# Kernel tuning notes

Measured on AMD Instinct MI355X. Metric: run time of the kernel, lower is better.

## Reference

```python
import jax, jax.numpy as jnp
import numpy as np

N = 100000   # number of points
K = 256      # num_clusters
F = 256      # num_features


def setup_inputs() -> dict:
    key = jax.random.key(0)
    k1, k2 = jax.random.split(key)
    x = jax.random.normal(k1, (1, N, F), dtype=jnp.float32)
    cluster_centers = jax.random.normal(k2, (K, F), dtype=jnp.float32)
    return {"x": x, "cluster_centers": cluster_centers}


def reference(x, cluster_centers):
    # x: (1, n, F); cluster_centers: (K, F)
    # Euclidean distances (1, n, K) via expansion (same math as norm of diff,
    # without materializing the (1, n, K, F) intermediate the torch code builds).
    x_sq = jnp.sum(x * x, axis=-1)                              # (1, n)
    c_sq = jnp.sum(cluster_centers * cluster_centers, axis=-1)  # (K,)
    cross = jnp.einsum('bnf,kf->bnk', x, cluster_centers)       # (1, n, K)
    d2 = x_sq[..., None] + c_sq[None, None, :] - 2.0 * cross
    distances = jnp.sqrt(jnp.maximum(d2, 0.0))                  # (1, n, K)
    # For each cluster, index of the nearest point (argmin over n).
    indices = jnp.argmin(distances, axis=1)                     # (1, K)
    # Gather the features of the nearest point per cluster.
    selected = jnp.take_along_axis(x, indices[:, :, None], axis=1)  # (1, K, F)
    return selected
```

## Files before the change

kernel.cpp:

```cpp
#include <hip/hip_runtime.h>
#include <stdint.h>

#define N_PTS 100000
#define K_CL  256
#define F_DIM 256
#define XROW  264

using bf16x8 = __attribute__((ext_vector_type(8))) short;
using f32x4  = __attribute__((ext_vector_type(4))) float;
typedef unsigned long long u64;

__device__ __forceinline__ unsigned short f32_to_bf16_rne(float f) {
    unsigned u = __float_as_uint(f);
    unsigned r = u + 0x7FFFu + ((u >> 16) & 1u);
    return (unsigned short)(r >> 16);
}

__global__ void prep_kernel(const float* __restrict__ c,
                            unsigned short* __restrict__ ch,
                            unsigned short* __restrict__ cl,
                            float* __restrict__ csq,
                            u64* __restrict__ best) {
    const int k = blockIdx.x;
    const int lane = threadIdx.x;
    float4 v = *(const float4*)(c + (size_t)k * F_DIM + lane * 4);

    float e[4] = {v.x, v.y, v.z, v.w};
    unsigned short hh[4], ll[4];
    #pragma unroll
    for (int i = 0; i < 4; ++i) {
        hh[i] = f32_to_bf16_rne(e[i]);
        float hf = __uint_as_float((unsigned)hh[i] << 16);
        ll[i] = f32_to_bf16_rne(e[i] - hf);
    }
    *(ushort4*)(ch + (size_t)k * F_DIM + lane * 4) = make_ushort4(hh[0], hh[1], hh[2], hh[3]);
    *(ushort4*)(cl + (size_t)k * F_DIM + lane * 4) = make_ushort4(ll[0], ll[1], ll[2], ll[3]);

    float s = v.x * v.x;
    s = fmaf(v.y, v.y, s);
    s = fmaf(v.z, v.z, s);
    s = fmaf(v.w, v.w, s);
    #pragma unroll
    for (int off = 32; off; off >>= 1) s += __shfl_down(s, off, 64);
    if (lane == 0) { csq[k] = s; best[k] = 0xFFFFFFFFFFFFFFFFULL; }
}

__global__ __launch_bounds__(512, 4)
void cluster_argmin_kernel(const float* __restrict__ x,
                           const unsigned short* __restrict__ ch,
                           const unsigned short* __restrict__ cl,
                           const float* __restrict__ csq,
                           u64* __restrict__ best) {
    __shared__ unsigned short xh_lds[64][XROW];
    __shared__ unsigned short xl_lds[64][XROW];
    __shared__ float xsq_lds[64];

    const int tid  = threadIdx.x;
    const int lane = tid & 63;
    const int w    = __builtin_amdgcn_readfirstlane(tid >> 6);
    const int n0   = blockIdx.x * 64;
    const int r15  = lane & 15;
    const int kg   = lane >> 4;

    const int col = lane * 4;
    #pragma unroll
    for (int i = 0; i < 8; ++i) {
        const int row = w + i * 8;
        int gr = n0 + row; if (gr > N_PTS - 1) gr = N_PTS - 1;
        float4 v = *(const float4*)(x + (size_t)gr * F_DIM + col);
        unsigned short h4[4], l4[4];
        float e[4] = {v.x, v.y, v.z, v.w};
        float s = 0.f;
        #pragma unroll
        for (int j = 0; j < 4; ++j) {
            h4[j] = f32_to_bf16_rne(e[j]);
            float hf = __uint_as_float((unsigned)h4[j] << 16);
            l4[j] = f32_to_bf16_rne(e[j] - hf);
            s = fmaf(e[j], e[j], s);
        }
        *(ushort4*)&xh_lds[row][col] = make_ushort4(h4[0], h4[1], h4[2], h4[3]);
        *(ushort4*)&xl_lds[row][col] = make_ushort4(l4[0], l4[1], l4[2], l4[3]);
        #pragma unroll
        for (int off = 32; off; off >>= 1) s += __shfl_xor(s, off, 64);
        if (lane == 0) xsq_lds[row] = s;
    }
    __syncthreads();

    const int kb = w * 32;
    const unsigned short* cbh[2];
    const unsigned short* cbl[2];
    #pragma unroll
    for (int cg = 0; cg < 2; ++cg) {
        size_t off = (size_t)(kb + cg * 16 + r15) * F_DIM + kg * 8;
        cbh[cg] = ch + off;
        cbl[cg] = cl + off;
    }

    f32x4 acc[4][2];
    #pragma unroll
    for (int pg = 0; pg < 4; ++pg)
        #pragma unroll
        for (int cg = 0; cg < 2; ++cg)
            acc[pg][cg] = (f32x4){0.f, 0.f, 0.f, 0.f};

    #pragma unroll 2
    for (int it = 0; it < 8; ++it) {
        const int f0 = it * 32;
        bf16x8 bh[2], bl[2];
        #pragma unroll
        for (int cg = 0; cg < 2; ++cg) {
            bh[cg] = *(const bf16x8*)(cbh[cg] + f0);
            bl[cg] = *(const bf16x8*)(cbl[cg] + f0);
        }
        #pragma unroll
        for (int pg = 0; pg < 4; ++pg) {
            bf16x8 xh8 = *(const bf16x8*)&xh_lds[pg * 16 + r15][f0 + kg * 8];
            bf16x8 xl8 = *(const bf16x8*)&xl_lds[pg * 16 + r15][f0 + kg * 8];
            #pragma unroll
            for (int cg = 0; cg < 2; ++cg) {
                acc[pg][cg] = __builtin_amdgcn_mfma_f32_16x16x32_bf16(
                    xh8, bh[cg], acc[pg][cg], 0, 0, 0);
                acc[pg][cg] = __builtin_amdgcn_mfma_f32_16x16x32_bf16(
                    xh8, bl[cg], acc[pg][cg], 0, 0, 0);
                acc[pg][cg] = __builtin_amdgcn_mfma_f32_16x16x32_bf16(
                    xl8, bh[cg], acc[pg][cg], 0, 0, 0);
            }
        }
    }

    u64 keep = 0xFFFFFFFFFFFFFFFFULL;
    #pragma unroll
    for (int cg = 0; cg < 2; ++cg) {
        const float cs = csq[kb + cg * 16 + r15];
        u64 m = 0xFFFFFFFFFFFFFFFFULL;
        #pragma unroll
        for (int pg = 0; pg < 4; ++pg) {
            #pragma unroll
            for (int r = 0; r < 4; ++r) {
                const int pl = pg * 16 + kg * 4 + r;
                const int n  = n0 + pl;
                float d2 = fmaf(-2.f, acc[pg][cg][r], xsq_lds[pl] + cs);
                d2 = fmaxf(d2, 0.f);
                float d = sqrtf(d2);
                u64 pk = ((u64)__float_as_uint(d) << 32) | (unsigned)n;
                if (n >= N_PTS) pk = 0xFFFFFFFFFFFFFFFFULL;
                m = pk < m ? pk : m;
            }
        }
        u64 o = __shfl_xor(m, 16, 64); m = o < m ? o : m;
        o = __shfl_xor(m, 32, 64);     m = o < m ? o : m;
        if (kg == cg) keep = m;
    }
    if (lane < 32) {
        u64 cur = best[kb + lane];
        if (keep < cur) atomicMin(&best[kb + lane], keep);
    }
}

__global__ void gather_kernel(const float* __restrict__ x,
                              const u64* __restrict__ best,
                              float* __restrict__ out) {
    int k = blockIdx.x;
    unsigned int idx = (unsigned int)(best[k] & 0xFFFFFFFFULL);
    int t = threadIdx.x;
    float4 v = *(const float4*)(x + (size_t)idx * F_DIM + t * 4);
    *(float4*)(out + (size_t)k * F_DIM + t * 4) = v;
}

extern "C" void kernel_launch(void* const* d_in, const int* in_sizes, int n_in,
                              void* d_out, int out_size, void* d_ws, size_t ws_size,
                              hipStream_t stream) {
    const float* x = (const float*)d_in[0];
    const float* c = (const float*)d_in[1];
    float* out = (float*)d_out;

    u64* best  = (u64*)d_ws;
    float* csq = (float*)((char*)d_ws + K_CL * sizeof(u64));

    unsigned short* ch = (unsigned short*)d_out;
    unsigned short* cl = ch + (size_t)K_CL * F_DIM;

    prep_kernel<<<K_CL, 64, 0, stream>>>(c, ch, cl, csq, best);

    int nblocks = (N_PTS + 63) / 64;
    cluster_argmin_kernel<<<nblocks, 512, 0, stream>>>(x, ch, cl, csq, best);

    gather_kernel<<<K_CL, 64, 0, stream>>>(x, best, out);
}
```

Baseline: 217.4 us.

## Pre-swizzle centroid fragments and XOR-swizzle LDS tiles for MFMA loads

The prep kernel now writes the centroid hi/lo bf16 splits in MFMA fragment order, so each lane reads one contiguous 16-byte chunk per step and global loads coalesce fully. The x tile in LDS drops the padded rows for a rotated chunk swizzle, meant to avoid bank conflicts on the bf16x8 reads. The main kernel also issues all eight row loads before converting, uses packed bf16 conversion intrinsics, groups the LDS reads ahead of the MFMA block, and raises wave priority around the MFMAs. The trade-off is more registers held per thread and more intricate indexing that has to match exactly between the prep and consumer kernels.

```diff
diff --git a/kernel.cpp b/kernel.cpp
--- a/kernel.cpp
+++ b/kernel.cpp
@@ -1,58 +1,64 @@
 #include <hip/hip_runtime.h>
+#include <hip/hip_bf16.h>
 #include <stdint.h>
 
 #define N_PTS 100000
 #define K_CL  256
 #define F_DIM 256
-#define XROW  264
 
 using bf16x8 = __attribute__((ext_vector_type(8))) short;
 using f32x4  = __attribute__((ext_vector_type(4))) float;
 typedef unsigned long long u64;
 
-__device__ __forceinline__ unsigned short f32_to_bf16_rne(float f) {
-    unsigned u = __float_as_uint(f);
-    unsigned r = u + 0x7FFFu + ((u >> 16) & 1u);
-    return (unsigned short)(r >> 16);
+__device__ __forceinline__ unsigned pk2(float a, float b) {
+    __hip_bfloat162 h = __float22bfloat162_rn(make_float2(a, b));
+    unsigned u;
+    __builtin_memcpy(&u, &h, 4);
+    return u;
 }
 
 __global__ void prep_kernel(const float* __restrict__ c,
-                            unsigned short* __restrict__ ch,
-                            unsigned short* __restrict__ cl,
+                            unsigned short* __restrict__ chf,
+                            unsigned short* __restrict__ clf,
                             float* __restrict__ csq,
                             u64* __restrict__ best) {
     const int k = blockIdx.x;
     const int lane = threadIdx.x;
-    float4 v = *(const float4*)(c + (size_t)k * F_DIM + lane * 4);
-
-    float e[4] = {v.x, v.y, v.z, v.w};
-    unsigned short hh[4], ll[4];
-    #pragma unroll
-    for (int i = 0; i < 4; ++i) {
-        hh[i] = f32_to_bf16_rne(e[i]);
-        float hf = __uint_as_float((unsigned)hh[i] << 16);
-        ll[i] = f32_to_bf16_rne(e[i] - hf);
-    }
-    *(ushort4*)(ch + (size_t)k * F_DIM + lane * 4) = make_ushort4(hh[0], hh[1], hh[2], hh[3]);
-    *(ushort4*)(cl + (size_t)k * F_DIM + lane * 4) = make_ushort4(ll[0], ll[1], ll[2], ll[3]);
-
-    float s = v.x * v.x;
-    s = fmaf(v.y, v.y, s);
-    s = fmaf(v.z, v.z, s);
-    s = fmaf(v.w, v.w, s);
-    #pragma unroll
-    for (int off = 32; off; off >>= 1) s += __shfl_down(s, off, 64);
+    float s = 0.f;
+    if (lane < 32) {
+        const int b = lane;
+        const float* src = c + (size_t)k * F_DIM + b * 8;
+        float4 v0 = *(const float4*)(src);
+        float4 v1 = *(const float4*)(src + 4);
+        float e[8] = {v0.x, v0.y, v0.z, v0.w, v1.x, v1.y, v1.z, v1.w};
+        unsigned h[4], l[4];
+        #pragma unroll
+        for (int j = 0; j < 4; ++j) {
+            h[j] = pk2(e[2 * j], e[2 * j + 1]);
+            float r0 = e[2 * j]     - __uint_as_float(h[j] << 16);
+            float r1 = e[2 * j + 1] - __uint_as_float(h[j] & 0xFFFF0000u);
+            l[j] = pk2(r0, r1);
+            s = fmaf(e[2 * j], e[2 * j], s);
+            s = fmaf(e[2 * j + 1], e[2 * j + 1], s);
+        }
+        const size_t fi = ((size_t)(k >> 4) * 8 + (b >> 2)) * 64
+                        + (b & 3) * 16 + (k & 15);
+        *(uint4*)(chf + fi * 8) = make_uint4(h[0], h[1], h[2], h[3]);
+        *(uint4*)(clf + fi * 8) = make_uint4(l[0], l[1], l[2], l[3]);
+    }
+    #pragma unroll
+    for (int off = 16; off; off >>= 1) s += __shfl_down(s, off, 64);
     if (lane == 0) { csq[k] = s; best[k] = 0xFFFFFFFFFFFFFFFFULL; }
 }
 
 __global__ __launch_bounds__(512, 4)
 void cluster_argmin_kernel(const float* __restrict__ x,
-                           const unsigned short* __restrict__ ch,
-                           const unsigned short* __restrict__ cl,
+                           const unsigned short* __restrict__ chf,
+                           const unsigned short* __restrict__ clf,
                            const float* __restrict__ csq,
                            u64* __restrict__ best) {
-    __shared__ unsigned short xh_lds[64][XROW];
-    __shared__ unsigned short xl_lds[64][XROW];
+    __shared__ unsigned short xh_lds[64 * 256];
+    __shared__ unsigned short xl_lds[64 * 256];
     __shared__ float xsq_lds[64];
 
     const int tid  = threadIdx.x;
@@ -62,24 +68,33 @@
     const int r15  = lane & 15;
     const int kg   = lane >> 4;
 
-    const int col = lane * 4;
+    float4 v[8];
+    #pragma unroll
+    for (int i = 0; i < 8; ++i) {
+        int gr = n0 + w + i * 8;
+        if (gr > N_PTS - 1) gr = N_PTS - 1;
+        v[i] = *(const float4*)(x + (size_t)gr * F_DIM + lane * 4);
+    }
     #pragma unroll
     for (int i = 0; i < 8; ++i) {
         const int row = w + i * 8;
-        int gr = n0 + row; if (gr > N_PTS - 1) gr = N_PTS - 1;
-        float4 v = *(const float4*)(x + (size_t)gr * F_DIM + col);
-        unsigned short h4[4], l4[4];
-        float e[4] = {v.x, v.y, v.z, v.w};
-        float s = 0.f;
-        #pragma unroll
-        for (int j = 0; j < 4; ++j) {
-            h4[j] = f32_to_bf16_rne(e[j]);
-            float hf = __uint_as_float((unsigned)h4[j] << 16);
-            l4[j] = f32_to_bf16_rne(e[j] - hf);
-            s = fmaf(e[j], e[j], s);
-        }
-        *(ushort4*)&xh_lds[row][col] = make_ushort4(h4[0], h4[1], h4[2], h4[3]);
-        *(ushort4*)&xl_lds[row][col] = make_ushort4(l4[0], l4[1], l4[2], l4[3]);
+        float e[4] = {v[i].x, v[i].y, v[i].z, v[i].w};
+        unsigned h01 = pk2(e[0], e[1]);
+        unsigned h23 = pk2(e[2], e[3]);
+        float r0 = e[0] - __uint_as_float(h01 << 16);
+        float r1 = e[1] - __uint_as_float(h01 & 0xFFFF0000u);
+        float r2 = e[2] - __uint_as_float(h23 << 16);
+        float r3 = e[3] - __uint_as_float(h23 & 0xFFFF0000u);
+        unsigned l01 = pk2(r0, r1);
+        unsigned l23 = pk2(r2, r3);
+        const int p = ((lane >> 1) + 2 * row) & 31;
+        const int so = row * 256 + p * 8 + (lane & 1) * 4;
+        *(uint2*)&xh_lds[so] = make_uint2(h01, h23);
+        *(uint2*)&xl_lds[so] = make_uint2(l01, l23);
+        float s = fmaf(e[0], e[0], 0.f);
+        s = fmaf(e[1], e[1], s);
+        s = fmaf(e[2], e[2], s);
+        s = fmaf(e[3], e[3], s);
         #pragma unroll
         for (int off = 32; off; off >>= 1) s += __shfl_xor(s, off, 64);
         if (lane == 0) xsq_lds[row] = s;
@@ -87,14 +102,10 @@
     __syncthreads();
 
     const int kb = w * 32;
-    const unsigned short* cbh[2];
-    const unsigned short* cbl[2];
-    #pragma unroll
-    for (int cg = 0; cg < 2; ++cg) {
-        size_t off = (size_t)(kb + cg * 16 + r15) * F_DIM + kg * 8;
-        cbh[cg] = ch + off;
-        cbl[cg] = cl + off;
-    }
+    const unsigned short* fh0 = chf + ((size_t)(2 * w)     * 8) * 64 * 8 + lane * 8;
+    const unsigned short* fh1 = chf + ((size_t)(2 * w + 1) * 8) * 64 * 8 + lane * 8;
+    const unsigned short* fl0 = clf + ((size_t)(2 * w)     * 8) * 64 * 8 + lane * 8;
+    const unsigned short* fl1 = clf + ((size_t)(2 * w + 1) * 8) * 64 * 8 + lane * 8;
 
     f32x4 acc[4][2];
     #pragma unroll
@@ -105,27 +116,35 @@
 
     #pragma unroll 2
     for (int it = 0; it < 8; ++it) {
-        const int f0 = it * 32;
         bf16x8 bh[2], bl[2];
-        #pragma unroll
-        for (int cg = 0; cg < 2; ++cg) {
-            bh[cg] = *(const bf16x8*)(cbh[cg] + f0);
-            bl[cg] = *(const bf16x8*)(cbl[cg] + f0);
-        }
+        bh[0] = *(const bf16x8*)(fh0 + (size_t)it * 512);
+        bh[1] = *(const bf16x8*)(fh1 + (size_t)it * 512);
+        bl[0] = *(const bf16x8*)(fl0 + (size_t)it * 512);
+        bl[1] = *(const bf16x8*)(fl1 + (size_t)it * 512);
+
+        bf16x8 xh8[4], xl8[4];
         #pragma unroll
         for (int pg = 0; pg < 4; ++pg) {
-            bf16x8 xh8 = *(const bf16x8*)&xh_lds[pg * 16 + r15][f0 + kg * 8];
-            bf16x8 xl8 = *(const bf16x8*)&xl_lds[pg * 16 + r15][f0 + kg * 8];
+            const int row = pg * 16 + r15;
+            const int p = (4 * it + kg + 2 * row) & 31;
+            const int so = row * 256 + p * 8;
+            xh8[pg] = *(const bf16x8*)&xh_lds[so];
+            xl8[pg] = *(const bf16x8*)&xl_lds[so];
+        }
+        __builtin_amdgcn_s_setprio(1);
+        #pragma unroll
+        for (int pg = 0; pg < 4; ++pg) {
             #pragma unroll
             for (int cg = 0; cg < 2; ++cg) {
                 acc[pg][cg] = __builtin_amdgcn_mfma_f32_16x16x32_bf16(
-                    xh8, bh[cg], acc[pg][cg], 0, 0, 0);
+                    xh8[pg], bh[cg], acc[pg][cg], 0, 0, 0);
                 acc[pg][cg] = __builtin_amdgcn_mfma_f32_16x16x32_bf16(
-                    xh8, bl[cg], acc[pg][cg], 0, 0, 0);
+                    xh8[pg], bl[cg], acc[pg][cg], 0, 0, 0);
                 acc[pg][cg] = __builtin_amdgcn_mfma_f32_16x16x32_bf16(
-                    xl8, bh[cg], acc[pg][cg], 0, 0, 0);
+                    xl8[pg], bh[cg], acc[pg][cg], 0, 0, 0);
             }
         }
+        __builtin_amdgcn_s_setprio(0);
     }
 
     u64 keep = 0xFFFFFFFFFFFFFFFFULL;
@@ -177,13 +196,13 @@
     u64* best  = (u64*)d_ws;
     float* csq = (float*)((char*)d_ws + K_CL * sizeof(u64));
 
-    unsigned short* ch = (unsigned short*)d_out;
-    unsigned short* cl = ch + (size_t)K_CL * F_DIM;
-
-    prep_kernel<<<K_CL, 64, 0, stream>>>(c, ch, cl, csq, best);
+    unsigned short* chf = (unsigned short*)d_out;
+    unsigned short* clf = chf + (size_t)K_CL * F_DIM;
+
+    prep_kernel<<<K_CL, 64, 0, stream>>>(c, chf, clf, csq, best);
 
     int nblocks = (N_PTS + 63) / 64;
-    cluster_argmin_kernel<<<nblocks, 512, 0, stream>>>(x, ch, cl, csq, best);
+    cluster_argmin_kernel<<<nblocks, 512, 0, stream>>>(x, chf, clf, csq, best);
 
     gather_kernel<<<K_CL, 64, 0, stream>>>(x, best, out);
 }
```

Result: faster. 190.5 us (-12.4%).
